# Kernel tuning notes

Measured on AMD Instinct MI355X. Metric: run time of the kernel, lower is better.

The kernel has to match this reference:

```python
import jax, jax.numpy as jnp
import numpy as np

EPS = 1e-6
NUM_SPECIAL = 4
NUM_HEADS = 16


def _rms_norm(x, w, eps=EPS):
    # x: [..., d], normalize over last dim
    var = jnp.mean(jnp.square(x), axis=-1, keepdims=True)
    return x * jax.lax.rsqrt(var + eps) * w


def _rotate_half(x):
    d = x.shape[-1] // 2
    return jnp.concatenate([-x[..., d:], x[..., :d]], axis=-1)


def _apply_rotary(q, k, cos, sin):
    # q,k: [B,H,N,hd]; cos,sin: [N,hd] -> broadcast [1,1,N,hd]
    cos = cos[None, None, :, :]
    sin = sin[None, None, :, :]
    q_out = q * cos + _rotate_half(q) * sin
    k_out = k * cos + _rotate_half(k) * sin
    return q_out, k_out


def _make_2d_mask(seq_len, num_special, window):
    # special tokens attend / are attended fully; patches use 2D local box
    patch_len = seq_len - num_special
    gs = int(round(patch_len ** 0.5))
    idx = jnp.arange(seq_len)
    special = idx < num_special
    p = idx - num_special
    row = p // gs
    col = p % gs
    special_case = special[:, None] | special[None, :]
    swa = (jnp.abs(row[:, None] - row[None, :]) <= window) & (
        jnp.abs(col[:, None] - col[None, :]) <= window)
    return special_case | swa  # [N, N] bool


def setup_inputs() -> dict:
    key = jax.random.key(0)
    ks = jax.random.split(key, 7)
    B, N, C = 4, 1028, 1024
    hd = C // NUM_HEADS
    return {
        "hidden_states": jax.random.normal(ks[0], (B, N, C), dtype=jnp.float32),
        "cos": jax.random.uniform(ks[1], (N, hd), dtype=jnp.float32),
        "sin": jax.random.uniform(ks[2], (N, hd), dtype=jnp.float32),
        "qkv_w": jax.random.normal(ks[3], (3 * C, C), dtype=jnp.float32) * (C ** -0.5),
        "out_w": jax.random.normal(ks[4], (C, C), dtype=jnp.float32) * (C ** -0.5),
        "norm_q_w": jnp.ones((hd,), dtype=jnp.float32),
        "norm_k_w": jnp.ones((hd,), dtype=jnp.float32),
        "sliding_window": 2,
    }


def reference(hidden_states, cos, sin, qkv_w, out_w, norm_q_w, norm_k_w, sliding_window):
    B, N, C = hidden_states.shape
    H = NUM_HEADS
    hd = C // H

    # fused QKV projection (nn.Linear: x @ W^T)
    qkv = jnp.einsum('bnc,dc->bnd', hidden_states, qkv_w)
    qkv = qkv.reshape(B, N, 3, H, hd).transpose(2, 0, 3, 1, 4)  # [3,B,H,N,hd]
    q, k, v = qkv[0], qkv[1], qkv[2]

    # per-head-dim RMSNorm on q and k
    q = _rms_norm(q, norm_q_w)
    k = _rms_norm(k, norm_k_w)

    # RoPE
    q, k = _apply_rotary(q, k, cos, sin)

    # 2D sliding-window + special-token mask
    mask = _make_2d_mask(N, NUM_SPECIAL, sliding_window)  # [N,N]

    scale = 1.0 / jnp.sqrt(jnp.asarray(hd, dtype=q.dtype))
    scores = jnp.einsum('bhqd,bhkd->bhqk', q, k) * scale
    neg = jnp.asarray(jnp.finfo(scores.dtype).min, dtype=scores.dtype)
    scores = jnp.where(mask[None, None, :, :], scores, neg)
    probs = jax.nn.softmax(scores, axis=-1)
    attn = jnp.einsum('bhqk,bhkd->bhqd', probs, v)  # [B,H,N,hd]

    attn = attn.transpose(0, 2, 1, 3).reshape(B, N, C)
    return jnp.einsum('bnc,dc->bnd', attn, out_w)
```

## Files before the change

### kernel.cpp

```cpp
#include <hip/hip_runtime.h>
#include <hip/hip_bf16.h>
#include <stdint.h>

typedef __bf16 bf16;
typedef __attribute__((ext_vector_type(8))) __bf16 bf16x8;
typedef __attribute__((ext_vector_type(4))) __bf16 bf16x4;
typedef __attribute__((ext_vector_type(4))) float f32x4;

#define NSEQ 1028
#define CDIM 1024
#define NHEADS 16
#define HD 64
#define BHN 64
#define NPAD 1088
#define M_REAL 4112
#define MTILES 33

static __device__ __forceinline__ void async_copy16(bf16* lds, const bf16* g) {
  __builtin_amdgcn_global_load_lds(
      (const __attribute__((address_space(1))) uint32_t*)g,
      (__attribute__((address_space(3))) uint32_t*)lds, 16, 0, 0);
}

__global__ __launch_bounds__(256) void cast3_kernel(
    const float* __restrict__ s0, bf16* __restrict__ d0, long n0,
    const float* __restrict__ s1, bf16* __restrict__ d1, long n1,
    const float* __restrict__ s2, bf16* __restrict__ d2, long n2) {
  long total = n0 + n1 + n2;
  long t = (long)blockIdx.x * 256 + threadIdx.x;
  long stride = (long)gridDim.x * 256;
  for (long j = t * 4; j < total; j += stride * 4) {
    const float* s; bf16* d; long jj = j;
    if (jj < n0) { s = s0; d = d0; }
    else if (jj < n0 + n1) { s = s1; d = d1; jj -= n0; }
    else { s = s2; d = d2; jj -= n0 + n1; }
    float4 v = *(const float4*)(s + jj);
    bf16x4 o;
    o[0] = (bf16)v.x; o[1] = (bf16)v.y; o[2] = (bf16)v.z; o[3] = (bf16)v.w;
    *(bf16x4*)(d + jj) = o;
  }
}

template <int EPI, int NSTRIP, int BN, int DEPTH>
__global__ __launch_bounds__(256, 4) void gemm_bf16_kernel(
    const bf16* __restrict__ A, const bf16* __restrict__ Bm,
    bf16* __restrict__ q_bf, bf16* __restrict__ k_bf, bf16* __restrict__ v_raw,
    float* __restrict__ outF,
    const float* __restrict__ cosb, const float* __restrict__ sinb,
    const float* __restrict__ nqw, const float* __restrict__ nkw) {
  constexpr int K = CDIM;
  constexpr int N = NSTRIP * 8 * BN;
  constexpr int HN = BN / 2;
  constexpr int NJ = HN / 16;
  constexpr int BSLOTS = (BN * 4) / 256;
  constexpr int LPS = 2 + BSLOTS;
  constexpr int NBUF = DEPTH + 1;
  __shared__ __attribute__((aligned(16))) bf16 As[NBUF][128 * 32];
  __shared__ __attribute__((aligned(16))) bf16 Bs[NBUF][BN * 32];
  const int tid = threadIdx.x;
  const int lane = tid & 63;
  const int wid = tid >> 6;
  const int wr = wid >> 1, wc = wid & 1;
  const int l15 = lane & 15, l4 = lane >> 4;

  const int xcd = blockIdx.x & 7;
  const int pos = blockIdx.x >> 3;
  const int nloc = pos % NSTRIP;
  const int mi = pos / NSTRIP;
  const int n0 = (xcd * NSTRIP + nloc) * BN;
  const int m0 = (mi < MTILES - 1) ? (mi << 7) : (M_REAL - 128);

  f32x4 acc[4][NJ] = {};

  size_t a_base[2], b_base[BSLOTS];
#pragma unroll
  for (int s = 0; s < 2; s++) {
    int c = tid + s * 256;
    int u = c ^ ((c >> 3) & 7);
    a_base[s] = (size_t)(m0 + (u >> 2)) * K + ((u & 3) << 3);
  }
#pragma unroll
  for (int s = 0; s < BSLOTS; s++) {
    int c = tid + s * 256;
    int u = c ^ ((c >> 3) & 7);
    b_base[s] = (size_t)(n0 + (u >> 2)) * K + ((u & 3) << 3);
  }

#define STAGE(bufi, ktof)                                                   \
  {                                                                         \
    _Pragma("unroll")                                                       \
    for (int s = 0; s < 2; s++)                                             \
      async_copy16(&As[bufi][(tid + s * 256) * 8], A + a_base[s] + (ktof)); \
    _Pragma("unroll")                                                       \
    for (int s = 0; s < BSLOTS; s++)                                        \
      async_copy16(&Bs[bufi][(tid + s * 256) * 8], Bm + b_base[s] + (ktof));\
  }

  const int nt = K >> 5;
#pragma unroll
  for (int d = 0; d < DEPTH; d++) STAGE(d, d << 5);

  for (int t = 0; t < nt; ++t) {
    if (t + DEPTH < nt) STAGE((t + DEPTH) % NBUF, (t + DEPTH) << 5);
    const int left = nt - 1 - t;
    if (left >= DEPTH) {
      asm volatile("s_waitcnt vmcnt(%0)" :: "i"(DEPTH * LPS) : "memory");
    } else if (left == 2) {
      asm volatile("s_waitcnt vmcnt(%0)" :: "i"(2 * LPS) : "memory");
    } else if (left == 1) {
      asm volatile("s_waitcnt vmcnt(%0)" :: "i"(LPS) : "memory");
    } else {
      asm volatile("s_waitcnt vmcnt(0)" ::: "memory");
    }
    __builtin_amdgcn_s_barrier();

    const int cur = t % NBUF;
    bf16x8 af[4], bfr[NJ];
#pragma unroll
    for (int i = 0; i < 4; i++) {
      int u = ((wr * 64 + i * 16 + l15) << 2) | l4;
      af[i] = *(const bf16x8*)&As[cur][(u ^ ((u >> 3) & 7)) << 3];
    }
#pragma unroll
    for (int j = 0; j < NJ; j++) {
      int u = ((wc * HN + j * 16 + l15) << 2) | l4;
      bfr[j] = *(const bf16x8*)&Bs[cur][(u ^ ((u >> 3) & 7)) << 3];
    }

#pragma unroll
    for (int i = 0; i < 4; i++)
#pragma unroll
      for (int j = 0; j < NJ; j++)
        acc[i][j] = __builtin_amdgcn_mfma_f32_16x16x32_bf16(af[i], bfr[j], acc[i][j], 0, 0, 0);

    asm volatile("s_waitcnt lgkmcnt(0)" ::: "memory");
    __builtin_amdgcn_s_barrier();
  }
#undef STAGE

  if (EPI == 0) {
    const int d_base = n0 + wc * 64;
    const int tsel = d_base >> 10;
    const int hh = (d_base & 1023) >> 6;
    if (tsel == 2) {
#pragma unroll
      for (int i = 0; i < 4; i++)
#pragma unroll
        for (int r = 0; r < 4; r++) {
          int m = m0 + wr * 64 + i * 16 + l4 * 4 + r;
          int b = m / NSEQ, n = m % NSEQ;
          size_t rb = ((size_t)(b * NHEADS + hh) * NSEQ + n) * HD;
#pragma unroll
          for (int j = 0; j < NJ; j++)
            v_raw[rb + j * 16 + l15] = (bf16)acc[i][j][r];
        }
    } else {
      const float* wn = (tsel == 0) ? nqw : nkw;
      bf16* dst = (tsel == 0) ? q_bf : k_bf;
      float wv[NJ];
#pragma unroll
      for (int j = 0; j < NJ; j++) wv[j] = wn[j * 16 + l15];
#pragma unroll
      for (int i = 0; i < 4; i++)
#pragma unroll
        for (int r = 0; r < 4; r++) {
          int m = m0 + wr * 64 + i * 16 + l4 * 4 + r;
          float ss = 0.0f;
#pragma unroll
          for (int j = 0; j < NJ; j++) { float x = acc[i][j][r]; ss += x * x; }
          ss += __shfl_xor(ss, 1);
          ss += __shfl_xor(ss, 2);
          ss += __shfl_xor(ss, 4);
          ss += __shfl_xor(ss, 8);
          float rms = rsqrtf(ss * (1.0f / HD) + 1e-6f);
          int b = m / NSEQ, n = m % NSEQ;
          float qn[NJ];
#pragma unroll
          for (int j = 0; j < NJ; j++) qn[j] = acc[i][j][r] * rms * wv[j];
          size_t rb = ((size_t)(b * NHEADS + hh) * NPAD + n) * HD;
#pragma unroll
          for (int j = 0; j < NJ; j++) {
            float c = cosb[n * HD + j * 16 + l15];
            float s = sinb[n * HD + j * 16 + l15];
            float rot = (j < 2) ? -qn[j + 2] : qn[j - 2];
            dst[rb + j * 16 + l15] = (bf16)(qn[j] * c + rot * s);
          }
        }
    }
  } else {
#pragma unroll
    for (int i = 0; i < 4; i++)
#pragma unroll
      for (int j = 0; j < NJ; j++) {
        int d = n0 + wc * HN + j * 16 + l15;
        int mrow = m0 + wr * 64 + i * 16 + l4 * 4;
#pragma unroll
        for (int r = 0; r < 4; r++) {
          int m = mrow + r;
          outF[(size_t)m * N + d] = acc[i][j][r];
        }
      }
  }
}

__global__ __launch_bounds__(256) void v_transpose_kernel(const bf16* __restrict__ v_raw,
                                                          bf16* __restrict__ vT) {
  __shared__ bf16 tile[64][65];
  int bh = blockIdx.y, c = blockIdx.x;
  int tid = threadIdx.x;
#pragma unroll
  for (int jj = 0; jj < 16; jj++) {
    int idx = tid + jj * 256;
    int i = idx >> 6, e = idx & 63;
    int n = (c == 0) ? i : (64 * c - 60 + i);
    bool ok = (c == 0) ? (i < 4) : (n < NSEQ);
    tile[i][e] = ok ? v_raw[((size_t)bh * NSEQ + n) * HD + e] : (bf16)0.0f;
  }
  __syncthreads();
#pragma unroll
  for (int jj = 0; jj < 16; jj++) {
    int idx = tid + jj * 256;
    int e = idx >> 6, i = idx & 63;
    vT[((size_t)bh * HD + e) * NPAD + 64 * c + i] = tile[i][e];
  }
}

__global__ __launch_bounds__(256) void attn_kernel(
    const bf16* __restrict__ Q, const bf16* __restrict__ Kb, const bf16* __restrict__ Vt,
    bf16* __restrict__ att, const int* __restrict__ winp) {
  __shared__ __attribute__((aligned(16))) bf16 P_s[4][16][72];
  __shared__ float o_s[4][4][64];
  __shared__ float ml_s[4][2][16];
  const int bh = blockIdx.y, qt = blockIdx.x;
  const int W = winp[0];
  const int tid = threadIdx.x, w = tid >> 6, lane = tid & 63;
  const int l15 = lane & 15, l4 = lane >> 4;
  const size_t qkbase = (size_t)bh * NPAD * HD;
  const size_t vtb = (size_t)bh * HD * NPAD;
  const bool is_spec = (qt == 16);

  const int qrow0 = is_spec ? 0 : (4 + qt * 64 + w * 16);
  bf16x8 aq0 = *(const bf16x8*)&Q[qkbase + (size_t)(qrow0 + l15) * HD + l4 * 8];
  bf16x8 aq1 = *(const bf16x8*)&Q[qkbase + (size_t)(qrow0 + l15) * HD + 32 + l4 * 8];

  float mrow[4], lrow[4];
  f32x4 o[4] = {};
#pragma unroll
  for (int r = 0; r < 4; r++) { mrow[r] = -1e30f; lrow[r] = 0.0f; }

  int p0, pstep, pmax, toff;
  if (is_spec) {
    p0 = w; pstep = 4; pmax = 16; toff = -1;
  } else {
    int ta = ((2 * qt - W + 64) >> 1) - 32;
    int tb = (2 * qt + 1 + W) >> 1;
    ta = ta < 0 ? 0 : ta;
    tb = tb > 15 ? 15 : tb;
    p0 = 0; pstep = 1; pmax = tb - ta + 1; toff = ta - 1;
  }

  for (int p = p0; p <= pmax; p += pstep) {
    const bool sp = (p == 0);
    const int tau = toff + p;
    const int krow0 = sp ? 0 : (4 + tau * 64);
    const int vcol0 = sp ? 0 : (64 + tau * 64);

    f32x4 sacc[4] = {};
#pragma unroll
    for (int kf = 0; kf < 4; kf++) {
      const bf16* kp = &Kb[qkbase + (size_t)(krow0 + kf * 16 + l15) * HD];
      bf16x8 b0 = *(const bf16x8*)(kp + l4 * 8);
      bf16x8 b1 = *(const bf16x8*)(kp + 32 + l4 * 8);
      sacc[kf] = __builtin_amdgcn_mfma_f32_16x16x32_bf16(aq0, b0, sacc[kf], 0, 0, 0);
      sacc[kf] = __builtin_amdgcn_mfma_f32_16x16x32_bf16(aq1, b1, sacc[kf], 0, 0, 0);
    }

    float pvv[4][4];
#pragma unroll
    for (int kf = 0; kf < 4; kf++)
#pragma unroll
      for (int r = 0; r < 4; r++) {
        float s = sacc[kf][r] * 0.125f;
        bool valid;
        if (sp) {
          valid = (kf == 0) && (l15 < 4);
        } else if (is_spec) {
          valid = true;
        } else {
          int p_k = tau * 64 + kf * 16 + l15;
          int p_q = qt * 64 + w * 16 + l4 * 4 + r;
          int dr = (p_q >> 5) - (p_k >> 5); dr = dr < 0 ? -dr : dr;
          int dc = (p_q & 31) - (p_k & 31); dc = dc < 0 ? -dc : dc;
          valid = (dr <= W) && (dc <= W);
        }
        pvv[kf][r] = valid ? s : -1e30f;
      }

#pragma unroll
    for (int r = 0; r < 4; r++) {
      float mx = fmaxf(fmaxf(pvv[0][r], pvv[1][r]), fmaxf(pvv[2][r], pvv[3][r]));
#pragma unroll
      for (int mm = 1; mm < 16; mm <<= 1) mx = fmaxf(mx, __shfl_xor(mx, mm));
      float mnew = fmaxf(mrow[r], mx);
      float scale = __expf(mrow[r] - mnew);
      float rs = 0.0f;
#pragma unroll
      for (int kf = 0; kf < 4; kf++) {
        float pp = __expf(pvv[kf][r] - mnew);
        pvv[kf][r] = pp;
        rs += pp;
      }
#pragma unroll
      for (int mm = 1; mm < 16; mm <<= 1) rs += __shfl_xor(rs, mm);
      lrow[r] = lrow[r] * scale + rs;
      mrow[r] = mnew;
#pragma unroll
      for (int f = 0; f < 4; f++) o[f][r] *= scale;
    }

#pragma unroll
    for (int kf = 0; kf < 4; kf++)
#pragma unroll
      for (int r = 0; r < 4; r++)
        P_s[w][l4 * 4 + r][kf * 16 + l15] = (bf16)pvv[kf][r];

    bf16x8 pa0 = *(const bf16x8*)&P_s[w][l15][l4 * 8];
    bf16x8 pa1 = *(const bf16x8*)&P_s[w][l15][32 + l4 * 8];
#pragma unroll
    for (int f = 0; f < 4; f++) {
      const bf16* vp = &Vt[vtb + (size_t)(f * 16 + l15) * NPAD + vcol0];
      bf16x8 v0 = *(const bf16x8*)(vp + l4 * 8);
      bf16x8 v1 = *(const bf16x8*)(vp + 32 + l4 * 8);
      o[f] = __builtin_amdgcn_mfma_f32_16x16x32_bf16(pa0, v0, o[f], 0, 0, 0);
      o[f] = __builtin_amdgcn_mfma_f32_16x16x32_bf16(pa1, v1, o[f], 0, 0, 0);
    }
  }

  const int b = bh >> 4, h = bh & 15;
  if (!is_spec) {
#pragma unroll
    for (int f = 0; f < 4; f++)
#pragma unroll
      for (int r = 0; r < 4; r++) {
        int n = qrow0 + l4 * 4 + r;
        att[((size_t)(b * NSEQ + n)) * CDIM + h * HD + f * 16 + l15] =
            (bf16)(o[f][r] / lrow[r]);
      }
  } else {
    if (l4 == 0) {
#pragma unroll
      for (int f = 0; f < 4; f++)
#pragma unroll
        for (int r = 0; r < 4; r++) o_s[w][r][f * 16 + l15] = o[f][r];
      if (l15 == 0)
#pragma unroll
        for (int r = 0; r < 4; r++) { ml_s[w][0][r] = mrow[r]; ml_s[w][1][r] = lrow[r]; }
    }
    __syncthreads();
    int row = tid >> 6, dim = tid & 63;
    float M = -1e30f;
#pragma unroll
    for (int ww = 0; ww < 4; ww++) M = fmaxf(M, ml_s[ww][0][row]);
    float L = 0.0f, val = 0.0f;
#pragma unroll
    for (int ww = 0; ww < 4; ww++) {
      float e = __expf(ml_s[ww][0][row] - M);
      L += e * ml_s[ww][1][row];
      val += e * o_s[ww][row][dim];
    }
    att[((size_t)(b * NSEQ + row)) * CDIM + h * HD + dim] = (bf16)(val / L);
  }
}

extern "C" void kernel_launch(void* const* d_in, const int* in_sizes, int n_in,
                              void* d_out, int out_size, void* d_ws, size_t ws_size,
                              hipStream_t stream) {
  const float* hidden = (const float*)d_in[0];
  const float* cosb = (const float*)d_in[1];
  const float* sinb = (const float*)d_in[2];
  const float* qkv_w = (const float*)d_in[3];
  const float* out_w = (const float*)d_in[4];
  const float* norm_q_w = (const float*)d_in[5];
  const float* norm_k_w = (const float*)d_in[6];
  const int* win = (const int*)d_in[7];
  float* out = (float*)d_out;

  char* ws = (char*)d_ws;
  size_t off = 0;
  auto alloc = [&](size_t bytes) {
    char* p = ws + off;
    off += (bytes + 255) & ~(size_t)255;
    return p;
  };
  bf16* A_bf  = (bf16*)alloc((size_t)M_REAL * CDIM * 2);
  bf16* W1    = (bf16*)alloc((size_t)3 * CDIM * CDIM * 2);
  bf16* W2    = (bf16*)alloc((size_t)CDIM * CDIM * 2);
  bf16* v_raw = (bf16*)alloc((size_t)BHN * NSEQ * HD * 2);
  bf16* q_bf  = (bf16*)alloc((size_t)BHN * NPAD * HD * 2);
  bf16* k_bf  = (bf16*)alloc((size_t)BHN * NPAD * HD * 2);
  bf16* vT    = (bf16*)alloc((size_t)BHN * HD * NPAD * 2);
  bf16* att   = (bf16*)alloc((size_t)M_REAL * CDIM * 2);
  (void)ws_size; (void)in_sizes; (void)n_in; (void)out_size;

  cast3_kernel<<<2048, 256, 0, stream>>>(
      hidden, A_bf, (long)M_REAL * CDIM,
      qkv_w, W1, (long)3 * CDIM * CDIM,
      out_w, W2, (long)CDIM * CDIM);

  gemm_bf16_kernel<0, 3, 128, 1><<<792, 256, 0, stream>>>(
      A_bf, W1, q_bf, k_bf, v_raw, nullptr, cosb, sinb, norm_q_w, norm_k_w);
  v_transpose_kernel<<<dim3(17, 64), 256, 0, stream>>>(v_raw, vT);
  attn_kernel<<<dim3(17, 64), 256, 0, stream>>>(q_bf, k_bf, vT, att, win);
  gemm_bf16_kernel<1, 2, 64, 2><<<528, 256, 0, stream>>>(
      att, W2, nullptr, nullptr, nullptr, out, nullptr, nullptr, nullptr, nullptr);
}
```

Before: 129.1 us.

## Stage K/V tiles into double-buffered LDS via async copies in attention

In the non-special attention path, each K and V^T tile is now loaded once per block into double-buffered, XOR-swizzled LDS with async global-to-LDS copies, prefetching the next tile while computing the current one. Previously every wave loaded its own copy of K/V from global memory. The special-token path keeps direct global loads and reuses the KV buffer for its cross-wave reduction. The change also alters the GEMM wait-count ladder and a template argument of the output-projection GEMM, and it adds block barriers per iteration.

```diff
diff --git a/kernel.cpp b/kernel.cpp
--- a/kernel.cpp
+++ b/kernel.cpp
@@ -105,8 +105,6 @@
     const int left = nt - 1 - t;
     if (left >= DEPTH) {
       asm volatile("s_waitcnt vmcnt(%0)" :: "i"(DEPTH * LPS) : "memory");
-    } else if (left == 2) {
-      asm volatile("s_waitcnt vmcnt(%0)" :: "i"(2 * LPS) : "memory");
     } else if (left == 1) {
       asm volatile("s_waitcnt vmcnt(%0)" :: "i"(LPS) : "memory");
     } else {
@@ -229,8 +227,7 @@
     const bf16* __restrict__ Q, const bf16* __restrict__ Kb, const bf16* __restrict__ Vt,
     bf16* __restrict__ att, const int* __restrict__ winp) {
   __shared__ __attribute__((aligned(16))) bf16 P_s[4][16][72];
-  __shared__ float o_s[4][4][64];
-  __shared__ float ml_s[4][2][16];
+  __shared__ __attribute__((aligned(16))) bf16 KV[2][2][64 * 64];
   const int bh = blockIdx.y, qt = blockIdx.x;
   const int W = winp[0];
   const int tid = threadIdx.x, w = tid >> 6, lane = tid & 63;
@@ -238,6 +235,7 @@
   const size_t qkbase = (size_t)bh * NPAD * HD;
   const size_t vtb = (size_t)bh * HD * NPAD;
   const bool is_spec = (qt == 16);
+  const int b = bh >> 4, h = bh & 15;
 
   const int qrow0 = is_spec ? 0 : (4 + qt * 64 + w * 16);
   bf16x8 aq0 = *(const bf16x8*)&Q[qkbase + (size_t)(qrow0 + l15) * HD + l4 * 8];
@@ -248,96 +246,125 @@
 #pragma unroll
   for (int r = 0; r < 4; r++) { mrow[r] = -1e30f; lrow[r] = 0.0f; }
 
-  int p0, pstep, pmax, toff;
-  if (is_spec) {
-    p0 = w; pstep = 4; pmax = 16; toff = -1;
-  } else {
+  if (!is_spec) {
     int ta = ((2 * qt - W + 64) >> 1) - 32;
     int tb = (2 * qt + 1 + W) >> 1;
     ta = ta < 0 ? 0 : ta;
     tb = tb > 15 ? 15 : tb;
-    p0 = 0; pstep = 1; pmax = tb - ta + 1; toff = ta - 1;
-  }
-
-  for (int p = p0; p <= pmax; p += pstep) {
-    const bool sp = (p == 0);
-    const int tau = toff + p;
-    const int krow0 = sp ? 0 : (4 + tau * 64);
-    const int vcol0 = sp ? 0 : (64 + tau * 64);
-
-    f32x4 sacc[4] = {};
-#pragma unroll
-    for (int kf = 0; kf < 4; kf++) {
-      const bf16* kp = &Kb[qkbase + (size_t)(krow0 + kf * 16 + l15) * HD];
-      bf16x8 b0 = *(const bf16x8*)(kp + l4 * 8);
-      bf16x8 b1 = *(const bf16x8*)(kp + 32 + l4 * 8);
-      sacc[kf] = __builtin_amdgcn_mfma_f32_16x16x32_bf16(aq0, b0, sacc[kf], 0, 0, 0);
-      sacc[kf] = __builtin_amdgcn_mfma_f32_16x16x32_bf16(aq1, b1, sacc[kf], 0, 0, 0);
-    }
-
-    float pvv[4][4];
-#pragma unroll
-    for (int kf = 0; kf < 4; kf++)
+    const int P = tb - ta + 2;
+
+    int srow[2], sch[2];
+#pragma unroll
+    for (int s = 0; s < 2; s++) {
+      int c = tid + s * 256;
+      int u = c ^ ((c >> 3) & 7);
+      srow[s] = u >> 3; sch[s] = u & 7;
+    }
+
+#define STAGE_KV(bufi, p)                                                     \
+    {                                                                         \
+      int kr = (p) == 0 ? 0 : 4 + (ta + (p) - 1) * 64;                        \
+      int vc = (p) == 0 ? 0 : 64 + (ta + (p) - 1) * 64;                       \
+      _Pragma("unroll")                                                       \
+      for (int s = 0; s < 2; s++)                                             \
+        async_copy16(&KV[bufi][0][(tid + s * 256) * 8],                       \
+                     Kb + qkbase + (size_t)(kr + srow[s]) * HD + sch[s] * 8); \
+      _Pragma("unroll")                                                       \
+      for (int s = 0; s < 2; s++)                                             \
+        async_copy16(&KV[bufi][1][(tid + s * 256) * 8],                       \
+                     Vt + vtb + (size_t)srow[s] * NPAD + vc + sch[s] * 8);    \
+    }
+
+    STAGE_KV(0, 0);
+
+    for (int p = 0; p < P; ++p) {
+      if (p + 1 < P) {
+        STAGE_KV((p + 1) & 1, p + 1);
+        asm volatile("s_waitcnt vmcnt(4)" ::: "memory");
+      } else {
+        asm volatile("s_waitcnt vmcnt(0)" ::: "memory");
+      }
+      __builtin_amdgcn_s_barrier();
+
+      const int cur = p & 1;
+      const bool sp = (p == 0);
+      const int tau = ta + p - 1;
+
+      f32x4 sacc[4] = {};
+#pragma unroll
+      for (int kf = 0; kf < 4; kf++) {
+        int u0 = ((kf * 16 + l15) << 3) | l4;
+        int u1 = ((kf * 16 + l15) << 3) | (4 + l4);
+        bf16x8 b0 = *(const bf16x8*)&KV[cur][0][(u0 ^ ((u0 >> 3) & 7)) << 3];
+        bf16x8 b1 = *(const bf16x8*)&KV[cur][0][(u1 ^ ((u1 >> 3) & 7)) << 3];
+        sacc[kf] = __builtin_amdgcn_mfma_f32_16x16x32_bf16(aq0, b0, sacc[kf], 0, 0, 0);
+        sacc[kf] = __builtin_amdgcn_mfma_f32_16x16x32_bf16(aq1, b1, sacc[kf], 0, 0, 0);
+      }
+
+      float pvv[4][4];
+#pragma unroll
+      for (int kf = 0; kf < 4; kf++)
+#pragma unroll
+        for (int r = 0; r < 4; r++) {
+          float s = sacc[kf][r] * 0.125f;
+          bool valid;
+          if (sp) {
+            valid = (kf == 0) && (l15 < 4);
+          } else {
+            int p_k = tau * 64 + kf * 16 + l15;
+            int p_q = qt * 64 + w * 16 + l4 * 4 + r;
+            int dr = (p_q >> 5) - (p_k >> 5); dr = dr < 0 ? -dr : dr;
+            int dc = (p_q & 31) - (p_k & 31); dc = dc < 0 ? -dc : dc;
+            valid = (dr <= W) && (dc <= W);
+          }
+          pvv[kf][r] = valid ? s : -1e30f;
+        }
+
 #pragma unroll
       for (int r = 0; r < 4; r++) {
-        float s = sacc[kf][r] * 0.125f;
-        bool valid;
-        if (sp) {
-          valid = (kf == 0) && (l15 < 4);
-        } else if (is_spec) {
-          valid = true;
-        } else {
-          int p_k = tau * 64 + kf * 16 + l15;
-          int p_q = qt * 64 + w * 16 + l4 * 4 + r;
-          int dr = (p_q >> 5) - (p_k >> 5); dr = dr < 0 ? -dr : dr;
-          int dc = (p_q & 31) - (p_k & 31); dc = dc < 0 ? -dc : dc;
-          valid = (dr <= W) && (dc <= W);
-        }
-        pvv[kf][r] = valid ? s : -1e30f;
-      }
-
-#pragma unroll
-    for (int r = 0; r < 4; r++) {
-      float mx = fmaxf(fmaxf(pvv[0][r], pvv[1][r]), fmaxf(pvv[2][r], pvv[3][r]));
-#pragma unroll
-      for (int mm = 1; mm < 16; mm <<= 1) mx = fmaxf(mx, __shfl_xor(mx, mm));
-      float mnew = fmaxf(mrow[r], mx);
-      float scale = __expf(mrow[r] - mnew);
-      float rs = 0.0f;
-#pragma unroll
-      for (int kf = 0; kf < 4; kf++) {
-        float pp = __expf(pvv[kf][r] - mnew);
-        pvv[kf][r] = pp;
-        rs += pp;
-      }
-#pragma unroll
-      for (int mm = 1; mm < 16; mm <<= 1) rs += __shfl_xor(rs, mm);
-      lrow[r] = lrow[r] * scale + rs;
-      mrow[r] = mnew;
-#pragma unroll
-      for (int f = 0; f < 4; f++) o[f][r] *= scale;
-    }
-
-#pragma unroll
-    for (int kf = 0; kf < 4; kf++)
-#pragma unroll
-      for (int r = 0; r < 4; r++)
-        P_s[w][l4 * 4 + r][kf * 16 + l15] = (bf16)pvv[kf][r];
-
-    bf16x8 pa0 = *(const bf16x8*)&P_s[w][l15][l4 * 8];
-    bf16x8 pa1 = *(const bf16x8*)&P_s[w][l15][32 + l4 * 8];
-#pragma unroll
-    for (int f = 0; f < 4; f++) {
-      const bf16* vp = &Vt[vtb + (size_t)(f * 16 + l15) * NPAD + vcol0];
-      bf16x8 v0 = *(const bf16x8*)(vp + l4 * 8);
-      bf16x8 v1 = *(const bf16x8*)(vp + 32 + l4 * 8);
-      o[f] = __builtin_amdgcn_mfma_f32_16x16x32_bf16(pa0, v0, o[f], 0, 0, 0);
-      o[f] = __builtin_amdgcn_mfma_f32_16x16x32_bf16(pa1, v1, o[f], 0, 0, 0);
-    }
-  }
-
-  const int b = bh >> 4, h = bh & 15;
-  if (!is_spec) {
+        float mx = fmaxf(fmaxf(pvv[0][r], pvv[1][r]), fmaxf(pvv[2][r], pvv[3][r]));
+#pragma unroll
+        for (int mm = 1; mm < 16; mm <<= 1) mx = fmaxf(mx, __shfl_xor(mx, mm));
+        float mnew = fmaxf(mrow[r], mx);
+        float scale = __expf(mrow[r] - mnew);
+        float rs = 0.0f;
+#pragma unroll
+        for (int kf = 0; kf < 4; kf++) {
+          float pp = __expf(pvv[kf][r] - mnew);
+          pvv[kf][r] = pp;
+          rs += pp;
+        }
+#pragma unroll
+        for (int mm = 1; mm < 16; mm <<= 1) rs += __shfl_xor(rs, mm);
+        lrow[r] = lrow[r] * scale + rs;
+        mrow[r] = mnew;
+#pragma unroll
+        for (int f = 0; f < 4; f++) o[f][r] *= scale;
+      }
+
+#pragma unroll
+      for (int kf = 0; kf < 4; kf++)
+#pragma unroll
+        for (int r = 0; r < 4; r++)
+          P_s[w][l4 * 4 + r][kf * 16 + l15] = (bf16)pvv[kf][r];
+
+      bf16x8 pa0 = *(const bf16x8*)&P_s[w][l15][l4 * 8];
+      bf16x8 pa1 = *(const bf16x8*)&P_s[w][l15][32 + l4 * 8];
+#pragma unroll
+      for (int f = 0; f < 4; f++) {
+        int u0 = ((f * 16 + l15) << 3) | l4;
+        int u1 = ((f * 16 + l15) << 3) | (4 + l4);
+        bf16x8 v0 = *(const bf16x8*)&KV[cur][1][(u0 ^ ((u0 >> 3) & 7)) << 3];
+        bf16x8 v1 = *(const bf16x8*)&KV[cur][1][(u1 ^ ((u1 >> 3) & 7)) << 3];
+        o[f] = __builtin_amdgcn_mfma_f32_16x16x32_bf16(pa0, v0, o[f], 0, 0, 0);
+        o[f] = __builtin_amdgcn_mfma_f32_16x16x32_bf16(pa1, v1, o[f], 0, 0, 0);
+      }
+
+      asm volatile("s_waitcnt lgkmcnt(0)" ::: "memory");
+      __builtin_amdgcn_s_barrier();
+    }
+#undef STAGE_KV
+
 #pragma unroll
     for (int f = 0; f < 4; f++)
 #pragma unroll
@@ -347,26 +374,98 @@
             (bf16)(o[f][r] / lrow[r]);
       }
   } else {
+    float* o_sf = (float*)&KV[0][0][0];
+    float* ml_sf = o_sf + 4 * 4 * 64;
+
+    for (int p = w; p <= 16; p += 4) {
+      const bool sp = (p == 0);
+      const int tau = p - 1;
+      const int krow0 = sp ? 0 : (4 + tau * 64);
+      const int vcol0 = sp ? 0 : (64 + tau * 64);
+
+      f32x4 sacc[4] = {};
+#pragma unroll
+      for (int kf = 0; kf < 4; kf++) {
+        const bf16* kp = &Kb[qkbase + (size_t)(krow0 + kf * 16 + l15) * HD];
+        bf16x8 b0 = *(const bf16x8*)(kp + l4 * 8);
+        bf16x8 b1 = *(const bf16x8*)(kp + 32 + l4 * 8);
+        sacc[kf] = __builtin_amdgcn_mfma_f32_16x16x32_bf16(aq0, b0, sacc[kf], 0, 0, 0);
+        sacc[kf] = __builtin_amdgcn_mfma_f32_16x16x32_bf16(aq1, b1, sacc[kf], 0, 0, 0);
+      }
+
+      float pvv[4][4];
+#pragma unroll
+      for (int kf = 0; kf < 4; kf++)
+#pragma unroll
+        for (int r = 0; r < 4; r++) {
+          float s = sacc[kf][r] * 0.125f;
+          bool valid = sp ? ((kf == 0) && (l15 < 4)) : true;
+          pvv[kf][r] = valid ? s : -1e30f;
+        }
+
+#pragma unroll
+      for (int r = 0; r < 4; r++) {
+        float mx = fmaxf(fmaxf(pvv[0][r], pvv[1][r]), fmaxf(pvv[2][r], pvv[3][r]));
+#pragma unroll
+        for (int mm = 1; mm < 16; mm <<= 1) mx = fmaxf(mx, __shfl_xor(mx, mm));
+        float mnew = fmaxf(mrow[r], mx);
+        float scale = __expf(mrow[r] - mnew);
+        float rs = 0.0f;
+#pragma unroll
+        for (int kf = 0; kf < 4; kf++) {
+          float pp = __expf(pvv[kf][r] - mnew);
+          pvv[kf][r] = pp;
+          rs += pp;
+        }
+#pragma unroll
+        for (int mm = 1; mm < 16; mm <<= 1) rs += __shfl_xor(rs, mm);
+        lrow[r] = lrow[r] * scale + rs;
+        mrow[r] = mnew;
+#pragma unroll
+        for (int f = 0; f < 4; f++) o[f][r] *= scale;
+      }
+
+#pragma unroll
+      for (int kf = 0; kf < 4; kf++)
+#pragma unroll
+        for (int r = 0; r < 4; r++)
+          P_s[w][l4 * 4 + r][kf * 16 + l15] = (bf16)pvv[kf][r];
+
+      bf16x8 pa0 = *(const bf16x8*)&P_s[w][l15][l4 * 8];
+      bf16x8 pa1 = *(const bf16x8*)&P_s[w][l15][32 + l4 * 8];
+#pragma unroll
+      for (int f = 0; f < 4; f++) {
+        const bf16* vp = &Vt[vtb + (size_t)(f * 16 + l15) * NPAD + vcol0];
+        bf16x8 v0 = *(const bf16x8*)(vp + l4 * 8);
+        bf16x8 v1 = *(const bf16x8*)(vp + 32 + l4 * 8);
+        o[f] = __builtin_amdgcn_mfma_f32_16x16x32_bf16(pa0, v0, o[f], 0, 0, 0);
+        o[f] = __builtin_amdgcn_mfma_f32_16x16x32_bf16(pa1, v1, o[f], 0, 0, 0);
+      }
+    }
+
     if (l4 == 0) {
 #pragma unroll
       for (int f = 0; f < 4; f++)
 #pragma unroll
-        for (int r = 0; r < 4; r++) o_s[w][r][f * 16 + l15] = o[f][r];
+        for (int r = 0; r < 4; r++) o_sf[(w * 4 + r) * 64 + f * 16 + l15] = o[f][r];
       if (l15 == 0)
 #pragma unroll
-        for (int r = 0; r < 4; r++) { ml_s[w][0][r] = mrow[r]; ml_s[w][1][r] = lrow[r]; }
+        for (int r = 0; r < 4; r++) {
+          ml_sf[(w * 2 + 0) * 16 + r] = mrow[r];
+          ml_sf[(w * 2 + 1) * 16 + r] = lrow[r];
+        }
     }
     __syncthreads();
     int row = tid >> 6, dim = tid & 63;
     float M = -1e30f;
 #pragma unroll
-    for (int ww = 0; ww < 4; ww++) M = fmaxf(M, ml_s[ww][0][row]);
+    for (int ww = 0; ww < 4; ww++) M = fmaxf(M, ml_sf[(ww * 2) * 16 + row]);
     float L = 0.0f, val = 0.0f;
 #pragma unroll
     for (int ww = 0; ww < 4; ww++) {
-      float e = __expf(ml_s[ww][0][row] - M);
-      L += e * ml_s[ww][1][row];
-      val += e * o_s[ww][row][dim];
+      float e = __expf(ml_sf[(ww * 2) * 16 + row] - M);
+      L += e * ml_sf[(ww * 2 + 1) * 16 + row];
+      val += e * o_sf[(ww * 4 + row) * 64 + dim];
     }
     att[((size_t)(b * NSEQ + row)) * CDIM + h * HD + dim] = (bf16)(val / L);
   }
@@ -411,6 +510,6 @@
       A_bf, W1, q_bf, k_bf, v_raw, nullptr, cosb, sinb, norm_q_w, norm_k_w);
   v_transpose_kernel<<<dim3(17, 64), 256, 0, stream>>>(v_raw, vT);
   attn_kernel<<<dim3(17, 64), 256, 0, stream>>>(q_bf, k_bf, vT, att, win);
-  gemm_bf16_kernel<1, 2, 64, 2><<<528, 256, 0, stream>>>(
+  gemm_bf16_kernel<1, 2, 64, 1><<<528, 256, 0, stream>>>(
       att, W2, nullptr, nullptr, nullptr, out, nullptr, nullptr, nullptr, nullptr);
 }
```

Result: faster. 110.0 us (median of 2 runs) (-14.8%).
